# Kernel optimization log

Measured on AMD Instinct MI355X. Metric: run time of the kernel, lower is better.

The kernel has to match this reference:

```python
import jax, jax.numpy as jnp
import numpy as np

N, E, F_IN, HID, L, G = 50000, 800000, 128, 64, 3, 512
BN_EPS = 1e-5


def setup_inputs() -> dict:
    key = jax.random.key(0)
    ks = jax.random.split(key, 8)
    x = jax.random.normal(ks[0], (N, F_IN), dtype=jnp.float32)
    edge_index = jax.random.randint(ks[1], (2, E), 0, N, dtype=jnp.int32)
    batch = jnp.sort(jax.random.randint(ks[2], (N,), 0, G, dtype=jnp.int32))
    # params (Glorot-ish init for weights; BN init per module: gamma=1, beta=1e-4)
    W_feat = jax.random.normal(ks[3], (F_IN, HID), dtype=jnp.float32) / np.sqrt(F_IN)
    b_feat = jnp.zeros((HID,), jnp.float32)
    Ws = jax.random.normal(ks[4], (L, HID, HID), dtype=jnp.float32) / np.sqrt(HID)
    bs = jnp.zeros((L, HID), jnp.float32)
    bn_feat_g = jnp.ones((F_IN,), jnp.float32)
    bn_feat_b = jnp.full((F_IN,), 1e-4, jnp.float32)
    bn_g = jnp.ones((L, HID), jnp.float32)
    bn_b = jnp.full((L, HID), 1e-4, jnp.float32)
    return {"x": x, "edge_index": edge_index, "batch": batch,
            "bn_feat_g": bn_feat_g, "bn_feat_b": bn_feat_b,
            "W_feat": W_feat, "b_feat": b_feat,
            "bn_g": bn_g, "bn_b": bn_b, "Ws": Ws, "bs": bs}


def batch_norm(x, gamma, beta):
    # training-mode BatchNorm1d: biased variance over the node dimension
    mu = jnp.mean(x, axis=0)
    var = jnp.mean(jnp.square(x - mu), axis=0)
    return (x - mu) * jax.lax.rsqrt(var + BN_EPS) * gamma + beta


def gcn_conv(h, W, b, src, dst):
    # h: [N, d_in] -> linear then normalized gather-scatter with self-loops
    h = h @ W  # [N, d_out]
    n = h.shape[0]
    loop = jnp.arange(n, dtype=src.dtype)
    row = jnp.concatenate([src, loop])  # source (j)
    col = jnp.concatenate([dst, loop])  # target (i)
    w = jnp.ones(row.shape[0], h.dtype)
    deg = jax.ops.segment_sum(w, row, num_segments=n)  # PyG: deg over row
    dis = jnp.where(deg > 0, jax.lax.rsqrt(jnp.maximum(deg, 1.0)), 0.0)
    norm = dis[row] * w * dis[col]  # [E+N]
    out = jax.ops.segment_sum(norm[:, None] * h[row], col, num_segments=n)
    return out + b


def reference(x, edge_index, batch, bn_feat_g, bn_feat_b, W_feat, b_feat,
              bn_g, bn_b, Ws, bs):
    src, dst = edge_index[0], edge_index[1]
    h = batch_norm(x, bn_feat_g, bn_feat_b)
    h = jax.nn.relu(h @ W_feat + b_feat)  # conv_feat has gfn=True -> plain linear
    for i in range(L):
        h = batch_norm(h, bn_g[i], bn_b[i])
        h = jax.nn.relu(gcn_conv(h, Ws[i], bs[i], src, dst))
    graph_emb = jax.ops.segment_sum(h, batch, num_segments=G)  # global_add_pool
    return graph_emb
```

## Files before the change

### kernel.cpp

```cpp
#include <hip/hip_runtime.h>
#include <math.h>

#define HID 64
#define BN_EPS 1e-5f
#define NBMAX 256
#define NREP 64

typedef unsigned int uint;
typedef unsigned short ushort;


__device__ inline uint bf16pk(float a, float b) {
    uint ua = __builtin_bit_cast(uint, a);
    ua += 0x7fff + ((ua >> 16) & 1);
    uint ub = __builtin_bit_cast(uint, b);
    ub += 0x7fff + ((ub >> 16) & 1);
    return (ua >> 16) | (ub & 0xffff0000u);
}
__device__ inline float bfl(uint v) { return __builtin_bit_cast(float, v << 16); }
__device__ inline float bfh(uint v) { return __builtin_bit_cast(float, v & 0xffff0000u); }


__global__ __launch_bounds__(256) void k_hist_scan(const int* __restrict__ ei, int E, int NB, int N,
                                                   int* __restrict__ bcnt_d, int* __restrict__ bcnt_s,
                                                   int* __restrict__ done,
                                                   int* __restrict__ bbase_d, int* __restrict__ cursor_d,
                                                   int* __restrict__ bbase_s, int* __restrict__ cursor_s,
                                                   int* __restrict__ rowptr) {
    __shared__ int hd[256], hs[256];
    __shared__ int lastFlag;
    int t = threadIdx.x;
    hd[t] = 0; hs[t] = 0;
    __syncthreads();
    for (int e = blockIdx.x * 256 + t; e < E; e += gridDim.x * 256) {
        int src = ei[e], dst = ei[E + e];
        atomicAdd(&hs[src >> 8], 1);
        atomicAdd(&hd[dst >> 8], 1);
    }
    __syncthreads();
    if (t < NB) {
        if (hd[t]) atomicAdd(&bcnt_d[t], hd[t]);
        if (hs[t]) atomicAdd(&bcnt_s[t], hs[t]);
    }
    __threadfence();
    __syncthreads();
    if (t == 0) lastFlag = (atomicAdd(done, 1) == (int)gridDim.x - 1);
    __syncthreads();
    if (!lastFlag) return;
    int v = (t < NB) ? atomicAdd(&bcnt_d[t], 0) : 0;
    hd[t] = v; __syncthreads();
    for (int s = 1; s < 256; s <<= 1) { int u = (t >= s) ? hd[t - s] : 0; __syncthreads(); hd[t] += u; __syncthreads(); }
    int excl = hd[t] - v;
    if (t <= NB) bbase_d[t] = excl;
    if (t < NB) cursor_d[t] = excl;
    if (t == 0) rowptr[N] = E;
    __syncthreads();
    v = (t < NB) ? atomicAdd(&bcnt_s[t], 0) : 0;
    hs[t] = v; __syncthreads();
    for (int s = 1; s < 256; s <<= 1) { int u = (t >= s) ? hs[t - s] : 0; __syncthreads(); hs[t] += u; __syncthreads(); }
    excl = hs[t] - v;
    if (t <= NB) bbase_s[t] = excl;
    if (t < NB) cursor_s[t] = excl;
}

__global__ __launch_bounds__(256) void k_scatter_stats(const int* __restrict__ ei, int E, int NB, int SCB,
                                                       int* __restrict__ cursor_d, int* __restrict__ cursor_s,
                                                       uint* __restrict__ bedge, int* __restrict__ bsrc,
                                                       const float* __restrict__ X, int n,
                                                       float* __restrict__ stats) {
    __shared__ __align__(16) char smemraw[8192];
    int t = threadIdx.x;
    if ((int)blockIdx.x < SCB) {
        int* hd = (int*)smemraw;
        int* hs = hd + 256;
        int* curd = hs + 256;
        int* curs = curd + 256;
        int chunk = (E + SCB - 1) / SCB;
        int e0 = blockIdx.x * chunk;
        int e1 = min(e0 + chunk, E);
        if (t < NB) { hd[t] = 0; hs[t] = 0; }
        __syncthreads();
        for (int e = e0 + t; e < e1; e += 256) {
            int src = ei[e], dst = ei[E + e];
            atomicAdd(&hd[dst >> 8], 1);
            atomicAdd(&hs[src >> 8], 1);
        }
        __syncthreads();
        if (t < NB) {
            curd[t] = hd[t] ? atomicAdd(&cursor_d[t], hd[t]) : 0;
            curs[t] = hs[t] ? atomicAdd(&cursor_s[t], hs[t]) : 0;
        }
        __syncthreads();
        for (int e = e0 + t; e < e1; e += 256) {
            int src = ei[e], dst = ei[E + e];
            int pd = atomicAdd(&curd[dst >> 8], 1);
            bedge[pd] = ((uint)(dst & 255) << 16) | (uint)src;
            int ps = atomicAdd(&curs[src >> 8], 1);
            bsrc[ps] = src;
        }
    } else {
        int b = blockIdx.x - SCB;
        int SB = gridDim.x - SCB;
        float4* shs = (float4*)smemraw;
        float4* shq = shs + 256;
        int c4 = t & 31, rsub = t >> 5;
        float4 s = make_float4(0.f, 0.f, 0.f, 0.f);
        float4 q = make_float4(0.f, 0.f, 0.f, 0.f);
        for (int r = b * 8 + rsub; r < n; r += SB * 8) {
            float4 v = ((const float4*)X)[(size_t)r * 32 + c4];
            s.x += v.x; s.y += v.y; s.z += v.z; s.w += v.w;
            q.x = fmaf(v.x, v.x, q.x); q.y = fmaf(v.y, v.y, q.y);
            q.z = fmaf(v.z, v.z, q.z); q.w = fmaf(v.w, v.w, q.w);
        }
        shs[t] = s; shq[t] = q;
        __syncthreads();
        if (rsub == 0) {
            #pragma unroll
            for (int k = 1; k < 8; k++) {
                float4 a = shs[t + k * 32], bq = shq[t + k * 32];
                s.x += a.x; s.y += a.y; s.z += a.z; s.w += a.w;
                q.x += bq.x; q.y += bq.y; q.z += bq.z; q.w += bq.w;
            }
            float* sb = stats + ((int)blockIdx.x & (NREP - 1)) * 256;
            atomicAdd(&sb[4 * t + 0], s.x); atomicAdd(&sb[4 * t + 1], s.y);
            atomicAdd(&sb[4 * t + 2], s.z); atomicAdd(&sb[4 * t + 3], s.w);
            atomicAdd(&sb[128 + 4 * t + 0], q.x); atomicAdd(&sb[128 + 4 * t + 1], q.y);
            atomicAdd(&sb[128 + 4 * t + 2], q.z); atomicAdd(&sb[128 + 4 * t + 3], q.w);
        }
    }
}

__global__ __launch_bounds__(256) void k_build_csr_outdeg(
        const uint* __restrict__ bedge, const int* __restrict__ bbase_d,
        const int* __restrict__ bsrc, const int* __restrict__ bbase_s,
        int N, int NB,
        int* __restrict__ rowptr, int* __restrict__ eidx, float* __restrict__ dis) {
    __shared__ int h[256], off[256], cur[256];
    int t = threadIdx.x, b = blockIdx.x;
    if (b < NB) {
        int base = bbase_d[b], end = bbase_d[b + 1];
        h[t] = 0; __syncthreads();
        for (int p = base + t; p < end; p += 256)
            atomicAdd(&h[(int)(bedge[p] >> 16) & 255], 1);
        __syncthreads();
        off[t] = h[t]; __syncthreads();
        for (int s = 1; s < 256; s <<= 1) { int u = (t >= s) ? off[t - s] : 0; __syncthreads(); off[t] += u; __syncthreads(); }
        int excl = off[t] - h[t];
        int node = (b << 8) + t;
        if (node <= N) rowptr[node] = base + excl;
        cur[t] = excl; __syncthreads();
        for (int p = base + t; p < end; p += 256) {
            uint be = bedge[p];
            int bin = (int)(be >> 16) & 255;
            int pos = atomicAdd(&cur[bin], 1);
            eidx[base + pos] = (int)(be & 0xffffu);
        }
    } else {
        int b2 = b - NB;
        int base = bbase_s[b2], end = bbase_s[b2 + 1];
        h[t] = 0; __syncthreads();
        for (int p = base + t; p < end; p += 256) atomicAdd(&h[bsrc[p] & 255], 1);
        __syncthreads();
        int node = (b2 << 8) + t;
        if (node < N) dis[node] = rsqrtf((float)(h[t] + 1));
    }
}


template <int K, bool RELU, bool DIS, bool STATS, bool HASB>
__global__ __launch_bounds__(256) void k_gemm(const float* __restrict__ X, const float* __restrict__ W,
                                              const float* __restrict__ stats,
                                              const float* __restrict__ gamma, const float* __restrict__ beta,
                                              const float* __restrict__ bias0, const float* __restrict__ dis,
                                              float n_inv, void* __restrict__ out, int n,
                                              float* __restrict__ sout) {
    constexpr int KC = 64;
    constexpr int XS = 68;
    __shared__ float Xs[KC * XS];
    __shared__ float Wsm[KC * HID];
    __shared__ float As[128], Cs[128];

    int t = threadIdx.x;
    int tx = t & 15, ty = t >> 4;
    int row0 = blockIdx.x * 64;

    if (t < K) {
        float ssum = 0.f, qsum = 0.f;
        const float* sp = stats + t;
        #pragma unroll 8
        for (int r = 0; r < NREP; ++r) {
            ssum += sp[(size_t)r * 2 * K];
            qsum += sp[(size_t)r * 2 * K + K];
        }
        float mu = ssum * n_inv;
        float var = qsum * n_inv - mu * mu;
        float a = gamma[t] * rsqrtf(var + BN_EPS);
        As[t] = a;
        Cs[t] = beta[t] - mu * a;
    }
    __syncthreads();

    float acc[4][4];
    #pragma unroll
    for (int i = 0; i < 4; i++)
        #pragma unroll
        for (int j = 0; j < 4; j++) acc[i][j] = 0.f;
    float4 bp = make_float4(0.f, 0.f, 0.f, 0.f);

    for (int kc = 0; kc < K; kc += KC) {
        #pragma unroll
        for (int it = 0; it < 4; ++it) {
            int id = t + 256 * it;
            int r = id >> 4, c4 = id & 15;
            float4 v = make_float4(0.f, 0.f, 0.f, 0.f);
            if (row0 + r < n) v = *(const float4*)(X + (size_t)(row0 + r) * K + kc + 4 * c4);
            int kk = 4 * c4;
            Xs[(kk + 0) * XS + r] = v.x;
            Xs[(kk + 1) * XS + r] = v.y;
            Xs[(kk + 2) * XS + r] = v.z;
            Xs[(kk + 3) * XS + r] = v.w;
        }
        {
            const float4* wsrc = (const float4*)(W + (size_t)kc * HID);
            #pragma unroll
            for (int it = 0; it < 4; ++it) {
                int id = t + 256 * it;
                int kl = id >> 4;
                float4 raw = wsrc[id];
                float a = As[kc + kl], c = Cs[kc + kl];
                float4 sc;
                sc.x = a * raw.x; sc.y = a * raw.y; sc.z = a * raw.z; sc.w = a * raw.w;
                ((float4*)Wsm)[id] = sc;
                bp.x = fmaf(c, raw.x, bp.x);
                bp.y = fmaf(c, raw.y, bp.y);
                bp.z = fmaf(c, raw.z, bp.z);
                bp.w = fmaf(c, raw.w, bp.w);
            }
        }
        __syncthreads();
        #pragma unroll 8
        for (int k = 0; k < KC; ++k) {
            float4 xv = *(const float4*)&Xs[k * XS + 4 * ty];
            float4 wv = *(const float4*)&Wsm[k * HID + 4 * tx];
            acc[0][0] = fmaf(xv.x, wv.x, acc[0][0]);
            acc[0][1] = fmaf(xv.x, wv.y, acc[0][1]);
            acc[0][2] = fmaf(xv.x, wv.z, acc[0][2]);
            acc[0][3] = fmaf(xv.x, wv.w, acc[0][3]);
            acc[1][0] = fmaf(xv.y, wv.x, acc[1][0]);
            acc[1][1] = fmaf(xv.y, wv.y, acc[1][1]);
            acc[1][2] = fmaf(xv.y, wv.z, acc[1][2]);
            acc[1][3] = fmaf(xv.y, wv.w, acc[1][3]);
            acc[2][0] = fmaf(xv.z, wv.x, acc[2][0]);
            acc[2][1] = fmaf(xv.z, wv.y, acc[2][1]);
            acc[2][2] = fmaf(xv.z, wv.z, acc[2][2]);
            acc[2][3] = fmaf(xv.z, wv.w, acc[2][3]);
            acc[3][0] = fmaf(xv.w, wv.x, acc[3][0]);
            acc[3][1] = fmaf(xv.w, wv.y, acc[3][1]);
            acc[3][2] = fmaf(xv.w, wv.z, acc[3][2]);
            acc[3][3] = fmaf(xv.w, wv.w, acc[3][3]);
        }
        __syncthreads();
    }

    {
        float* redb = Xs + 2048;
        *(float4*)&redb[ty * 64 + 4 * tx] = bp;
        __syncthreads();
        if (t < 64) {
            float s = 0.f;
            #pragma unroll
            for (int k = 0; k < 16; ++k) s += redb[k * 64 + t];
            Xs[3072 + t] = s + (HASB ? bias0[t] : 0.f);
        }
        __syncthreads();
    }
    float4 bv = *(const float4*)&Xs[3072 + 4 * tx];

    float4 cs = make_float4(0.f, 0.f, 0.f, 0.f);
    float4 cq = make_float4(0.f, 0.f, 0.f, 0.f);
    #pragma unroll
    for (int i = 0; i < 4; ++i) {
        int row = row0 + 4 * ty + i;
        bool valid = row < n;
        float vx = acc[i][0] + bv.x, vy = acc[i][1] + bv.y;
        float vz = acc[i][2] + bv.z, vw = acc[i][3] + bv.w;
        if constexpr (DIS) {
            if (valid) {
                float d = dis[row];
                uint2 pk;
                pk.x = bf16pk(vx * d, vy * d);
                pk.y = bf16pk(vz * d, vw * d);
                *(uint2*)((ushort*)out + (size_t)row * HID + 4 * tx) = pk;
            }
        } else {
            float4 v;
            v.x = RELU ? fmaxf(vx, 0.f) : vx;
            v.y = RELU ? fmaxf(vy, 0.f) : vy;
            v.z = RELU ? fmaxf(vz, 0.f) : vz;
            v.w = RELU ? fmaxf(vw, 0.f) : vw;
            if (valid) {
                *(float4*)((float*)out + (size_t)row * HID + 4 * tx) = v;
                if constexpr (STATS) {
                    cs.x += v.x; cs.y += v.y; cs.z += v.z; cs.w += v.w;
                    cq.x = fmaf(v.x, v.x, cq.x); cq.y = fmaf(v.y, v.y, cq.y);
                    cq.z = fmaf(v.z, v.z, cq.z); cq.w = fmaf(v.w, v.w, cq.w);
                }
            }
        }
    }
    if constexpr (STATS) {
        __syncthreads();
        float* reds = Xs;
        float* redq = Xs + 1024;
        *(float4*)&reds[ty * 64 + 4 * tx] = cs;
        *(float4*)&redq[ty * 64 + 4 * tx] = cq;
        __syncthreads();
        if (t < 64) {
            float s = 0.f, q = 0.f;
            #pragma unroll
            for (int k = 0; k < 16; ++k) { s += reds[k * 64 + t]; q += redq[k * 64 + t]; }
            float* sb = sout + ((int)blockIdx.x & (NREP - 1)) * 128;
            atomicAdd(&sb[t], s);
            atomicAdd(&sb[64 + t], q);
        }
    }
}


template <bool POOL>
__global__ __launch_bounds__(256) void k_agg(const ushort* __restrict__ s, const int* __restrict__ rowptr,
                                             const int* __restrict__ eidx, const float* __restrict__ dis,
                                             const float* __restrict__ bias, float* __restrict__ out, int n,
                                             float* __restrict__ sout, const int* __restrict__ batch,
                                             float* __restrict__ pool_out) {
    __shared__ float shs[8 * 64];
    __shared__ float shq[8 * 64];
    __shared__ int ib[8];
    int t = threadIdx.x;
    int nl = t >> 5;
    int li = t & 31;
    int slot = li >> 3;
    int c = li & 7;
    int i = blockIdx.x * 8 + nl;
    const uint4* sp4 = (const uint4*)s;
    float a[8];
    #pragma unroll
    for (int k = 0; k < 8; ++k) a[k] = 0.f;
    bool valid = i < n;
    if (valid) {
        int qe = rowptr[i + 1];
        int q = rowptr[i] + slot;
        while (q < qe) {
            int qm = qe - 1;
            int q1 = q + 4, q2 = q + 8, q3 = q + 12;
            bool p1 = q1 < qe, p2 = q2 < qe, p3 = q3 < qe;
            int j0 = eidx[q];
            int j1 = eidx[min(q1, qm)];
            int j2 = eidx[min(q2, qm)];
            int j3 = eidx[min(q3, qm)];
            if (!p1) j1 = i;
            if (!p2) j2 = i;
            if (!p3) j3 = i;
            uint4 v0 = sp4[(size_t)j0 * 8 + c];
            uint4 v1 = sp4[(size_t)j1 * 8 + c];
            uint4 v2 = sp4[(size_t)j2 * 8 + c];
            uint4 v3 = sp4[(size_t)j3 * 8 + c];
            float m1 = p1 ? 1.f : 0.f;
            float m2 = p2 ? 1.f : 0.f;
            float m3 = p3 ? 1.f : 0.f;
            q += 16;
            a[0] += bfl(v0.x); a[1] += bfh(v0.x);
            a[2] += bfl(v0.y); a[3] += bfh(v0.y);
            a[4] += bfl(v0.z); a[5] += bfh(v0.z);
            a[6] += bfl(v0.w); a[7] += bfh(v0.w);
            a[0] = fmaf(m1, bfl(v1.x), a[0]); a[1] = fmaf(m1, bfh(v1.x), a[1]);
            a[2] = fmaf(m1, bfl(v1.y), a[2]); a[3] = fmaf(m1, bfh(v1.y), a[3]);
            a[4] = fmaf(m1, bfl(v1.z), a[4]); a[5] = fmaf(m1, bfh(v1.z), a[5]);
            a[6] = fmaf(m1, bfl(v1.w), a[6]); a[7] = fmaf(m1, bfh(v1.w), a[7]);
            a[0] = fmaf(m2, bfl(v2.x), a[0]); a[1] = fmaf(m2, bfh(v2.x), a[1]);
            a[2] = fmaf(m2, bfl(v2.y), a[2]); a[3] = fmaf(m2, bfh(v2.y), a[3]);
            a[4] = fmaf(m2, bfl(v2.z), a[4]); a[5] = fmaf(m2, bfh(v2.z), a[5]);
            a[6] = fmaf(m2, bfl(v2.w), a[6]); a[7] = fmaf(m2, bfh(v2.w), a[7]);
            a[0] = fmaf(m3, bfl(v3.x), a[0]); a[1] = fmaf(m3, bfh(v3.x), a[1]);
            a[2] = fmaf(m3, bfl(v3.y), a[2]); a[3] = fmaf(m3, bfh(v3.y), a[3]);
            a[4] = fmaf(m3, bfl(v3.z), a[4]); a[5] = fmaf(m3, bfh(v3.z), a[5]);
            a[6] = fmaf(m3, bfl(v3.w), a[6]); a[7] = fmaf(m3, bfh(v3.w), a[7]);
        }
    }
    #pragma unroll
    for (int k = 0; k < 8; ++k) a[k] += __shfl_xor(a[k], 8);
    #pragma unroll
    for (int k = 0; k < 8; ++k) a[k] += __shfl_xor(a[k], 16);

    if (li < 8) {
        float r[8];
        if (valid) {
            uint4 v = sp4[(size_t)i * 8 + c];
            a[0] += bfl(v.x); a[1] += bfh(v.x);
            a[2] += bfl(v.y); a[3] += bfh(v.y);
            a[4] += bfl(v.z); a[5] += bfh(v.z);
            a[6] += bfl(v.w); a[7] += bfh(v.w);
            float d = dis[i];
            float4 b0 = *(const float4*)(bias + 8 * c);
            float4 b1 = *(const float4*)(bias + 8 * c + 4);
            r[0] = fmaxf(fmaf(d, a[0], b0.x), 0.f);
            r[1] = fmaxf(fmaf(d, a[1], b0.y), 0.f);
            r[2] = fmaxf(fmaf(d, a[2], b0.z), 0.f);
            r[3] = fmaxf(fmaf(d, a[3], b0.w), 0.f);
            r[4] = fmaxf(fmaf(d, a[4], b1.x), 0.f);
            r[5] = fmaxf(fmaf(d, a[5], b1.y), 0.f);
            r[6] = fmaxf(fmaf(d, a[6], b1.z), 0.f);
            r[7] = fmaxf(fmaf(d, a[7], b1.w), 0.f);
            if constexpr (!POOL) {
                *(float4*)(out + (size_t)i * HID + 8 * c)     = make_float4(r[0], r[1], r[2], r[3]);
                *(float4*)(out + (size_t)i * HID + 8 * c + 4) = make_float4(r[4], r[5], r[6], r[7]);
            }
        } else {
            #pragma unroll
            for (int k = 0; k < 8; ++k) r[k] = 0.f;
        }
        #pragma unroll
        for (int k = 0; k < 8; ++k) shs[nl * 64 + 8 * c + k] = r[k];
        if constexpr (!POOL) {
            #pragma unroll
            for (int k = 0; k < 8; ++k) shq[nl * 64 + 8 * c + k] = r[k] * r[k];
        }
    }
    if constexpr (POOL) {
        if (li == 0) ib[nl] = valid ? batch[i] : -1;
    }
    __syncthreads();
    if (t < 64) {
        if constexpr (!POOL) {
            float ss = 0.f, qq = 0.f;
            #pragma unroll
            for (int k = 0; k < 8; ++k) { ss += shs[k * 64 + t]; qq += shq[k * 64 + t]; }
            float* sb = sout + ((int)blockIdx.x & (NREP - 1)) * 128;
            atomicAdd(&sb[t], ss);
            atomicAdd(&sb[64 + t], qq);
        } else {
            int g = ib[0];
            float run = shs[t];
            #pragma unroll
            for (int k = 1; k < 8; ++k) {
                int gk = ib[k];
                float v = shs[k * 64 + t];
                if (gk == g) {
                    run += v;
                } else {
                    if (g >= 0) atomicAdd(&pool_out[(size_t)g * HID + t], run);
                    g = gk; run = v;
                }
            }
            if (g >= 0) atomicAdd(&pool_out[(size_t)g * HID + t], run);
        }
    }
}


extern "C" void kernel_launch(void* const* d_in, const int* in_sizes, int n_in,
                              void* d_out, int out_size, void* d_ws, size_t ws_size,
                              hipStream_t stream) {
    const float* x     = (const float*)d_in[0];
    const int*   ei    = (const int*)d_in[1];
    const int*   batch = (const int*)d_in[2];
    const float* bnfg  = (const float*)d_in[3];
    const float* bnfb  = (const float*)d_in[4];
    const float* Wfeat = (const float*)d_in[5];
    const float* bfeat = (const float*)d_in[6];
    const float* bng   = (const float*)d_in[7];
    const float* bnb   = (const float*)d_in[8];
    const float* Ws    = (const float*)d_in[9];
    const float* bs    = (const float*)d_in[10];
    float* out = (float*)d_out;

    const int N   = in_sizes[2];
    const int E   = in_sizes[1] / 2;
    const int L   = in_sizes[9] / (HID * HID);
    const int NB  = (N + 255) >> 8;
    const int SCB = 256;
    const int SB  = 512;
    const int gG  = (N + 63) / 64;
    const int gA  = (N + 7) / 8;
    const float n_inv = 1.f / (float)N;

    char* w = (char*)d_ws;
    auto alloc = [&](size_t bytes) { char* p = w; w += (bytes + 255) & ~(size_t)255; return p; };
    int*   bcnt_d = (int*)alloc(256 * 4);
    int*   bcnt_s = (int*)alloc(256 * 4);
    int*   done   = (int*)alloc(256);
    float* statsX = (float*)alloc((size_t)NREP * 256 * 4);
    float* statsL = (float*)alloc((size_t)3 * NREP * 128 * 4);
    size_t zero_bytes = (size_t)(w - (char*)d_ws);
    int*   bbase_d  = (int*)alloc(257 * 4);
    int*   cursor_d = (int*)alloc(256 * 4);
    int*   bbase_s  = (int*)alloc(257 * 4);
    int*   cursor_s = (int*)alloc(256 * 4);
    int*   rowptr   = (int*)alloc(((size_t)N + 1) * 4);
    int*   eidx     = (int*)alloc((size_t)E * 4);
    float* dis      = (float*)alloc((size_t)N * 4);
    float* bufA     = (float*)alloc((size_t)N * HID * 4);
    ushort* bufB    = (ushort*)alloc((size_t)N * HID * 2);
    uint* bedge = (uint*)bufA;
    int*  bsrc  = (int*)bufB;

    hipMemsetAsync(d_ws, 0, zero_bytes, stream);
    hipMemsetAsync(d_out, 0, (size_t)out_size * sizeof(float), stream);

    k_hist_scan<<<512, 256, 0, stream>>>(ei, E, NB, N, bcnt_d, bcnt_s, done,
                                         bbase_d, cursor_d, bbase_s, cursor_s, rowptr);
    k_scatter_stats<<<SCB + SB, 256, 0, stream>>>(ei, E, NB, SCB, cursor_d, cursor_s,
                                                  bedge, bsrc, x, N, statsX);
    k_build_csr_outdeg<<<2 * NB, 256, 0, stream>>>(bedge, bbase_d, bsrc, bbase_s, N, NB,
                                                   rowptr, eidx, dis);

    k_gemm<128, true, false, true, true><<<gG, 256, 0, stream>>>(
        x, Wfeat, statsX, bnfg, bnfb, bfeat, nullptr, n_inv, (void*)bufA, N, statsL);

    for (int l = 0; l < L; ++l) {
        k_gemm<64, false, true, false, false><<<gG, 256, 0, stream>>>(
            bufA, Ws + (size_t)l * HID * HID, statsL + (size_t)l * NREP * 128,
            bng + (size_t)l * HID, bnb + (size_t)l * HID,
            nullptr, dis, n_inv, (void*)bufB, N, nullptr);
        if (l < L - 1) {
            k_agg<false><<<gA, 256, 0, stream>>>(bufB, rowptr, eidx, dis, bs + (size_t)l * HID,
                                                 bufA, N, statsL + (size_t)(l + 1) * NREP * 128,
                                                 nullptr, nullptr);
        } else {
            k_agg<true><<<gA, 256, 0, stream>>>(bufB, rowptr, eidx, dis, bs + (size_t)l * HID,
                                                nullptr, N, nullptr, batch, out);
        }
    }
}
```

Measured before the change: 287.9 us.

## Build CSR with per-node atomic degrees, decoupled-lookback scan, and atomic fill

Replaces the two-level bucketed counting sort (bucket histogram, bucket scatter, per-bucket local sort) with a simpler CSR build. Per-node degrees now come from global atomics, a single-pass scan with decoupled lookback produces rowptr, cursor and dis, and an atomic-cursor fill writes eidx. This cuts the kernel count and the intermediate bedge/bsrc passes, at the cost of many contended global atomics. Edge order inside each row also becomes nondeterministic, so the aggregation's floating-point summation order can vary between runs.

```diff
diff --git a/kernel.cpp b/kernel.cpp
--- a/kernel.cpp
+++ b/kernel.cpp
@@ -3,7 +3,6 @@
 
 #define HID 64
 #define BN_EPS 1e-5f
-#define NBMAX 256
 #define NREP 64
 
 typedef unsigned int uint;
@@ -21,86 +20,22 @@
 __device__ inline float bfh(uint v) { return __builtin_bit_cast(float, v & 0xffff0000u); }
 
 
-__global__ __launch_bounds__(256) void k_hist_scan(const int* __restrict__ ei, int E, int NB, int N,
-                                                   int* __restrict__ bcnt_d, int* __restrict__ bcnt_s,
-                                                   int* __restrict__ done,
-                                                   int* __restrict__ bbase_d, int* __restrict__ cursor_d,
-                                                   int* __restrict__ bbase_s, int* __restrict__ cursor_s,
-                                                   int* __restrict__ rowptr) {
-    __shared__ int hd[256], hs[256];
-    __shared__ int lastFlag;
-    int t = threadIdx.x;
-    hd[t] = 0; hs[t] = 0;
-    __syncthreads();
-    for (int e = blockIdx.x * 256 + t; e < E; e += gridDim.x * 256) {
-        int src = ei[e], dst = ei[E + e];
-        atomicAdd(&hs[src >> 8], 1);
-        atomicAdd(&hd[dst >> 8], 1);
-    }
-    __syncthreads();
-    if (t < NB) {
-        if (hd[t]) atomicAdd(&bcnt_d[t], hd[t]);
-        if (hs[t]) atomicAdd(&bcnt_s[t], hs[t]);
-    }
-    __threadfence();
-    __syncthreads();
-    if (t == 0) lastFlag = (atomicAdd(done, 1) == (int)gridDim.x - 1);
-    __syncthreads();
-    if (!lastFlag) return;
-    int v = (t < NB) ? atomicAdd(&bcnt_d[t], 0) : 0;
-    hd[t] = v; __syncthreads();
-    for (int s = 1; s < 256; s <<= 1) { int u = (t >= s) ? hd[t - s] : 0; __syncthreads(); hd[t] += u; __syncthreads(); }
-    int excl = hd[t] - v;
-    if (t <= NB) bbase_d[t] = excl;
-    if (t < NB) cursor_d[t] = excl;
-    if (t == 0) rowptr[N] = E;
-    __syncthreads();
-    v = (t < NB) ? atomicAdd(&bcnt_s[t], 0) : 0;
-    hs[t] = v; __syncthreads();
-    for (int s = 1; s < 256; s <<= 1) { int u = (t >= s) ? hs[t - s] : 0; __syncthreads(); hs[t] += u; __syncthreads(); }
-    excl = hs[t] - v;
-    if (t <= NB) bbase_s[t] = excl;
-    if (t < NB) cursor_s[t] = excl;
-}
-
-__global__ __launch_bounds__(256) void k_scatter_stats(const int* __restrict__ ei, int E, int NB, int SCB,
-                                                       int* __restrict__ cursor_d, int* __restrict__ cursor_s,
-                                                       uint* __restrict__ bedge, int* __restrict__ bsrc,
-                                                       const float* __restrict__ X, int n,
-                                                       float* __restrict__ stats) {
+__global__ __launch_bounds__(256) void k_deg_stats(const int* __restrict__ ei, int E, int DB,
+                                                   int* __restrict__ deg_d, int* __restrict__ deg_s,
+                                                   const float* __restrict__ X, int n,
+                                                   float* __restrict__ stats) {
     __shared__ __align__(16) char smemraw[8192];
     int t = threadIdx.x;
-    if ((int)blockIdx.x < SCB) {
-        int* hd = (int*)smemraw;
-        int* hs = hd + 256;
-        int* curd = hs + 256;
-        int* curs = curd + 256;
-        int chunk = (E + SCB - 1) / SCB;
-        int e0 = blockIdx.x * chunk;
-        int e1 = min(e0 + chunk, E);
-        if (t < NB) { hd[t] = 0; hs[t] = 0; }
-        __syncthreads();
-        for (int e = e0 + t; e < e1; e += 256) {
+    if ((int)blockIdx.x < DB) {
+        int stride = DB * 256;
+        for (int e = blockIdx.x * 256 + t; e < E; e += stride) {
             int src = ei[e], dst = ei[E + e];
-            atomicAdd(&hd[dst >> 8], 1);
-            atomicAdd(&hs[src >> 8], 1);
-        }
-        __syncthreads();
-        if (t < NB) {
-            curd[t] = hd[t] ? atomicAdd(&cursor_d[t], hd[t]) : 0;
-            curs[t] = hs[t] ? atomicAdd(&cursor_s[t], hs[t]) : 0;
-        }
-        __syncthreads();
-        for (int e = e0 + t; e < e1; e += 256) {
-            int src = ei[e], dst = ei[E + e];
-            int pd = atomicAdd(&curd[dst >> 8], 1);
-            bedge[pd] = ((uint)(dst & 255) << 16) | (uint)src;
-            int ps = atomicAdd(&curs[src >> 8], 1);
-            bsrc[ps] = src;
+            atomicAdd(&deg_s[src], 1);
+            atomicAdd(&deg_d[dst], 1);
         }
     } else {
-        int b = blockIdx.x - SCB;
-        int SB = gridDim.x - SCB;
+        int b = blockIdx.x - DB;
+        int SB = gridDim.x - DB;
         float4* shs = (float4*)smemraw;
         float4* shq = shs + 256;
         int c4 = t & 31, rsub = t >> 5;
@@ -130,39 +65,80 @@
     }
 }
 
-__global__ __launch_bounds__(256) void k_build_csr_outdeg(
-        const uint* __restrict__ bedge, const int* __restrict__ bbase_d,
-        const int* __restrict__ bsrc, const int* __restrict__ bbase_s,
-        int N, int NB,
-        int* __restrict__ rowptr, int* __restrict__ eidx, float* __restrict__ dis) {
-    __shared__ int h[256], off[256], cur[256];
+
+__global__ __launch_bounds__(256) void k_scan_dis(const int* __restrict__ deg_d,
+                                                  const int* __restrict__ deg_s,
+                                                  int N, int E,
+                                                  int* __restrict__ rowptr, int* __restrict__ cursor,
+                                                  float* __restrict__ dis,
+                                                  int* __restrict__ aggr, int* __restrict__ flag) {
+    __shared__ int sh[256];
+    __shared__ int s_base;
     int t = threadIdx.x, b = blockIdx.x;
-    if (b < NB) {
-        int base = bbase_d[b], end = bbase_d[b + 1];
-        h[t] = 0; __syncthreads();
-        for (int p = base + t; p < end; p += 256)
-            atomicAdd(&h[(int)(bedge[p] >> 16) & 255], 1);
-        __syncthreads();
-        off[t] = h[t]; __syncthreads();
-        for (int s = 1; s < 256; s <<= 1) { int u = (t >= s) ? off[t - s] : 0; __syncthreads(); off[t] += u; __syncthreads(); }
-        int excl = off[t] - h[t];
-        int node = (b << 8) + t;
-        if (node <= N) rowptr[node] = base + excl;
-        cur[t] = excl; __syncthreads();
-        for (int p = base + t; p < end; p += 256) {
-            uint be = bedge[p];
-            int bin = (int)(be >> 16) & 255;
-            int pos = atomicAdd(&cur[bin], 1);
-            eidx[base + pos] = (int)(be & 0xffffu);
-        }
+    int base_el = b * 1024 + t * 4;
+
+    int4 ds = *(const int4*)(deg_s + base_el);
+    float4 dv;
+    dv.x = rsqrtf((float)(ds.x + 1)); dv.y = rsqrtf((float)(ds.y + 1));
+    dv.z = rsqrtf((float)(ds.z + 1)); dv.w = rsqrtf((float)(ds.w + 1));
+    if (base_el + 3 < N) *(float4*)(dis + base_el) = dv;
+    else {
+        if (base_el + 0 < N) dis[base_el + 0] = dv.x;
+        if (base_el + 1 < N) dis[base_el + 1] = dv.y;
+        if (base_el + 2 < N) dis[base_el + 2] = dv.z;
+        if (base_el + 3 < N) dis[base_el + 3] = dv.w;
+    }
+
+    int4 d = *(const int4*)(deg_d + base_el);
+    int s3 = d.x + d.y + d.z + d.w;
+    sh[t] = s3;
+    __syncthreads();
+    for (int off = 1; off < 256; off <<= 1) {
+        int u = (t >= off) ? sh[t - off] : 0;
+        __syncthreads();
+        sh[t] += u;
+        __syncthreads();
+    }
+    int excl_thread = sh[t] - s3;
+    int block_total = sh[255];
+
+    if (t == 0) {
+        s_base = 0;
+        atomicExch(&aggr[b], block_total);
+        __threadfence();
+        atomicExch(&flag[b], 1);
+    }
+    __syncthreads();
+    int lb = 0;
+    for (int p = t; p < b; p += 256) {
+        while (atomicAdd(&flag[p], 0) == 0) { __builtin_amdgcn_s_sleep(2); }
+        lb += atomicAdd(&aggr[p], 0);
+    }
+    if (lb) atomicAdd(&s_base, lb);
+    __syncthreads();
+
+    int base = s_base + excl_thread;
+    int r0 = base, r1 = r0 + d.x, r2 = r1 + d.y, r3 = r2 + d.z;
+    if (base_el + 3 < N) {
+        *(int4*)(rowptr + base_el) = make_int4(r0, r1, r2, r3);
+        *(int4*)(cursor + base_el) = make_int4(r0, r1, r2, r3);
     } else {
-        int b2 = b - NB;
-        int base = bbase_s[b2], end = bbase_s[b2 + 1];
-        h[t] = 0; __syncthreads();
-        for (int p = base + t; p < end; p += 256) atomicAdd(&h[bsrc[p] & 255], 1);
-        __syncthreads();
-        int node = (b2 << 8) + t;
-        if (node < N) dis[node] = rsqrtf((float)(h[t] + 1));
+        if (base_el + 0 < N) { rowptr[base_el + 0] = r0; cursor[base_el + 0] = r0; }
+        if (base_el + 1 < N) { rowptr[base_el + 1] = r1; cursor[base_el + 1] = r1; }
+        if (base_el + 2 < N) { rowptr[base_el + 2] = r2; cursor[base_el + 2] = r2; }
+        if (base_el + 3 < N) { rowptr[base_el + 3] = r3; cursor[base_el + 3] = r3; }
+    }
+    if (b == (int)gridDim.x - 1 && t == 255) rowptr[N] = E;
+}
+
+
+__global__ __launch_bounds__(256) void k_fill(const int* __restrict__ ei, int E,
+                                              int* __restrict__ cursor, int* __restrict__ eidx) {
+    int stride = gridDim.x * 256;
+    for (int e = blockIdx.x * 256 + threadIdx.x; e < E; e += stride) {
+        int src = ei[e], dst = ei[E + e];
+        int pos = atomicAdd(&cursor[dst], 1);
+        eidx[pos] = src;
     }
 }
 
@@ -477,42 +453,36 @@
     const int N   = in_sizes[2];
     const int E   = in_sizes[1] / 2;
     const int L   = in_sizes[9] / (HID * HID);
-    const int NB  = (N + 255) >> 8;
-    const int SCB = 256;
+    const int DB  = 512;
     const int SB  = 512;
+    const int SC  = (N + 1023) / 1024;
+    const int FB  = 1024;
     const int gG  = (N + 63) / 64;
     const int gA  = (N + 7) / 8;
     const float n_inv = 1.f / (float)N;
 
     char* w = (char*)d_ws;
     auto alloc = [&](size_t bytes) { char* p = w; w += (bytes + 255) & ~(size_t)255; return p; };
-    int*   bcnt_d = (int*)alloc(256 * 4);
-    int*   bcnt_s = (int*)alloc(256 * 4);
-    int*   done   = (int*)alloc(256);
+    int*   deg_d  = (int*)alloc(((size_t)N + 1024) * 4);
+    int*   deg_s  = (int*)alloc(((size_t)N + 1024) * 4);
+    int*   aggr   = (int*)alloc(256 * 4);
+    int*   flag   = (int*)alloc(256 * 4);
     float* statsX = (float*)alloc((size_t)NREP * 256 * 4);
     float* statsL = (float*)alloc((size_t)3 * NREP * 128 * 4);
     size_t zero_bytes = (size_t)(w - (char*)d_ws);
-    int*   bbase_d  = (int*)alloc(257 * 4);
-    int*   cursor_d = (int*)alloc(256 * 4);
-    int*   bbase_s  = (int*)alloc(257 * 4);
-    int*   cursor_s = (int*)alloc(256 * 4);
-    int*   rowptr   = (int*)alloc(((size_t)N + 1) * 4);
-    int*   eidx     = (int*)alloc((size_t)E * 4);
-    float* dis      = (float*)alloc((size_t)N * 4);
-    float* bufA     = (float*)alloc((size_t)N * HID * 4);
-    ushort* bufB    = (ushort*)alloc((size_t)N * HID * 2);
-    uint* bedge = (uint*)bufA;
-    int*  bsrc  = (int*)bufB;
+    int*   rowptr = (int*)alloc(((size_t)N + 1024) * 4);
+    int*   cursor = (int*)alloc(((size_t)N + 1024) * 4);
+    int*   eidx   = (int*)alloc((size_t)E * 4);
+    float* dis    = (float*)alloc((size_t)N * 4);
+    float* bufA   = (float*)alloc((size_t)N * HID * 4);
+    ushort* bufB  = (ushort*)alloc((size_t)N * HID * 2);
 
     hipMemsetAsync(d_ws, 0, zero_bytes, stream);
     hipMemsetAsync(d_out, 0, (size_t)out_size * sizeof(float), stream);
 
-    k_hist_scan<<<512, 256, 0, stream>>>(ei, E, NB, N, bcnt_d, bcnt_s, done,
-                                         bbase_d, cursor_d, bbase_s, cursor_s, rowptr);
-    k_scatter_stats<<<SCB + SB, 256, 0, stream>>>(ei, E, NB, SCB, cursor_d, cursor_s,
-                                                  bedge, bsrc, x, N, statsX);
-    k_build_csr_outdeg<<<2 * NB, 256, 0, stream>>>(bedge, bbase_d, bsrc, bbase_s, N, NB,
-                                                   rowptr, eidx, dis);
+    k_deg_stats<<<DB + SB, 256, 0, stream>>>(ei, E, DB, deg_d, deg_s, x, N, statsX);
+    k_scan_dis<<<SC, 256, 0, stream>>>(deg_d, deg_s, N, E, rowptr, cursor, dis, aggr, flag);
+    k_fill<<<FB, 256, 0, stream>>>(ei, E, cursor, eidx);
 
     k_gemm<128, true, false, true, true><<<gG, 256, 0, stream>>>(
         x, Wfeat, statsX, bnfg, bnfb, bfeat, nullptr, n_inv, (void*)bufA, N, statsL);
```

After: 345.4 us. 20.0% more time.

## Fuse input BN stats into histogram pass and first GEMM into edge scatter

Applied to the files above, without the earlier changes.

Moves the input-feature BatchNorm statistics reduction into the edge histogram/scan kernel, and runs the first feature GEMM in the same launch as the edge bucket scatter, using disjoint block ranges. This cuts one kernel launch and lets the independent graph-preprocessing and dense work overlap on the GPU. To allow the overlap, bedge/bsrc get their own workspace buffers instead of aliasing bufA/bufB, which costs extra memory. The combined kernel also uses more shared memory per block, which may lower occupancy for the scatter blocks.

```diff
diff --git a/kernel.cpp b/kernel.cpp
--- a/kernel.cpp
+++ b/kernel.cpp
@@ -3,7 +3,6 @@
 
 #define HID 64
 #define BN_EPS 1e-5f
-#define NBMAX 256
 #define NREP 64
 
 typedef unsigned int uint;
@@ -21,86 +20,53 @@
 __device__ inline float bfh(uint v) { return __builtin_bit_cast(float, v & 0xffff0000u); }
 
 
-__global__ __launch_bounds__(256) void k_hist_scan(const int* __restrict__ ei, int E, int NB, int N,
-                                                   int* __restrict__ bcnt_d, int* __restrict__ bcnt_s,
-                                                   int* __restrict__ done,
-                                                   int* __restrict__ bbase_d, int* __restrict__ cursor_d,
-                                                   int* __restrict__ bbase_s, int* __restrict__ cursor_s,
-                                                   int* __restrict__ rowptr) {
-    __shared__ int hd[256], hs[256];
+__global__ __launch_bounds__(256) void k_hist_scan_stats(
+        const int* __restrict__ ei, int E, int NB, int N, int HB,
+        int* __restrict__ bcnt_d, int* __restrict__ bcnt_s, int* __restrict__ done,
+        int* __restrict__ bbase_d, int* __restrict__ cursor_d,
+        int* __restrict__ bbase_s, int* __restrict__ cursor_s,
+        int* __restrict__ rowptr,
+        const float* __restrict__ X, int n, float* __restrict__ stats) {
+    __shared__ __align__(16) char smemraw[8192];
     __shared__ int lastFlag;
     int t = threadIdx.x;
-    hd[t] = 0; hs[t] = 0;
-    __syncthreads();
-    for (int e = blockIdx.x * 256 + t; e < E; e += gridDim.x * 256) {
-        int src = ei[e], dst = ei[E + e];
-        atomicAdd(&hs[src >> 8], 1);
-        atomicAdd(&hd[dst >> 8], 1);
-    }
-    __syncthreads();
-    if (t < NB) {
-        if (hd[t]) atomicAdd(&bcnt_d[t], hd[t]);
-        if (hs[t]) atomicAdd(&bcnt_s[t], hs[t]);
-    }
-    __threadfence();
-    __syncthreads();
-    if (t == 0) lastFlag = (atomicAdd(done, 1) == (int)gridDim.x - 1);
-    __syncthreads();
-    if (!lastFlag) return;
-    int v = (t < NB) ? atomicAdd(&bcnt_d[t], 0) : 0;
-    hd[t] = v; __syncthreads();
-    for (int s = 1; s < 256; s <<= 1) { int u = (t >= s) ? hd[t - s] : 0; __syncthreads(); hd[t] += u; __syncthreads(); }
-    int excl = hd[t] - v;
-    if (t <= NB) bbase_d[t] = excl;
-    if (t < NB) cursor_d[t] = excl;
-    if (t == 0) rowptr[N] = E;
-    __syncthreads();
-    v = (t < NB) ? atomicAdd(&bcnt_s[t], 0) : 0;
-    hs[t] = v; __syncthreads();
-    for (int s = 1; s < 256; s <<= 1) { int u = (t >= s) ? hs[t - s] : 0; __syncthreads(); hs[t] += u; __syncthreads(); }
-    excl = hs[t] - v;
-    if (t <= NB) bbase_s[t] = excl;
-    if (t < NB) cursor_s[t] = excl;
-}
-
-__global__ __launch_bounds__(256) void k_scatter_stats(const int* __restrict__ ei, int E, int NB, int SCB,
-                                                       int* __restrict__ cursor_d, int* __restrict__ cursor_s,
-                                                       uint* __restrict__ bedge, int* __restrict__ bsrc,
-                                                       const float* __restrict__ X, int n,
-                                                       float* __restrict__ stats) {
-    __shared__ __align__(16) char smemraw[8192];
-    int t = threadIdx.x;
-    if ((int)blockIdx.x < SCB) {
+    if ((int)blockIdx.x < HB) {
         int* hd = (int*)smemraw;
         int* hs = hd + 256;
-        int* curd = hs + 256;
-        int* curs = curd + 256;
-        int chunk = (E + SCB - 1) / SCB;
-        int e0 = blockIdx.x * chunk;
-        int e1 = min(e0 + chunk, E);
-        if (t < NB) { hd[t] = 0; hs[t] = 0; }
-        __syncthreads();
-        for (int e = e0 + t; e < e1; e += 256) {
+        hd[t] = 0; hs[t] = 0;
+        __syncthreads();
+        for (int e = blockIdx.x * 256 + t; e < E; e += HB * 256) {
             int src = ei[e], dst = ei[E + e];
+            atomicAdd(&hs[src >> 8], 1);
             atomicAdd(&hd[dst >> 8], 1);
-            atomicAdd(&hs[src >> 8], 1);
         }
         __syncthreads();
         if (t < NB) {
-            curd[t] = hd[t] ? atomicAdd(&cursor_d[t], hd[t]) : 0;
-            curs[t] = hs[t] ? atomicAdd(&cursor_s[t], hs[t]) : 0;
-        }
-        __syncthreads();
-        for (int e = e0 + t; e < e1; e += 256) {
-            int src = ei[e], dst = ei[E + e];
-            int pd = atomicAdd(&curd[dst >> 8], 1);
-            bedge[pd] = ((uint)(dst & 255) << 16) | (uint)src;
-            int ps = atomicAdd(&curs[src >> 8], 1);
-            bsrc[ps] = src;
-        }
+            if (hd[t]) atomicAdd(&bcnt_d[t], hd[t]);
+            if (hs[t]) atomicAdd(&bcnt_s[t], hs[t]);
+        }
+        __threadfence();
+        __syncthreads();
+        if (t == 0) lastFlag = (atomicAdd(done, 1) == HB - 1);
+        __syncthreads();
+        if (!lastFlag) return;
+        int v = (t < NB) ? atomicAdd(&bcnt_d[t], 0) : 0;
+        hd[t] = v; __syncthreads();
+        for (int s = 1; s < 256; s <<= 1) { int u = (t >= s) ? hd[t - s] : 0; __syncthreads(); hd[t] += u; __syncthreads(); }
+        int excl = hd[t] - v;
+        if (t <= NB) bbase_d[t] = excl;
+        if (t < NB) cursor_d[t] = excl;
+        if (t == 0) rowptr[N] = E;
+        __syncthreads();
+        v = (t < NB) ? atomicAdd(&bcnt_s[t], 0) : 0;
+        hs[t] = v; __syncthreads();
+        for (int s = 1; s < 256; s <<= 1) { int u = (t >= s) ? hs[t - s] : 0; __syncthreads(); hs[t] += u; __syncthreads(); }
+        excl = hs[t] - v;
+        if (t <= NB) bbase_s[t] = excl;
+        if (t < NB) cursor_s[t] = excl;
     } else {
-        int b = blockIdx.x - SCB;
-        int SB = gridDim.x - SCB;
+        int b = blockIdx.x - HB;
+        int SB = gridDim.x - HB;
         float4* shs = (float4*)smemraw;
         float4* shq = shs + 256;
         int c4 = t & 31, rsub = t >> 5;
@@ -130,50 +96,14 @@
     }
 }
 
-__global__ __launch_bounds__(256) void k_build_csr_outdeg(
-        const uint* __restrict__ bedge, const int* __restrict__ bbase_d,
-        const int* __restrict__ bsrc, const int* __restrict__ bbase_s,
-        int N, int NB,
-        int* __restrict__ rowptr, int* __restrict__ eidx, float* __restrict__ dis) {
-    __shared__ int h[256], off[256], cur[256];
-    int t = threadIdx.x, b = blockIdx.x;
-    if (b < NB) {
-        int base = bbase_d[b], end = bbase_d[b + 1];
-        h[t] = 0; __syncthreads();
-        for (int p = base + t; p < end; p += 256)
-            atomicAdd(&h[(int)(bedge[p] >> 16) & 255], 1);
-        __syncthreads();
-        off[t] = h[t]; __syncthreads();
-        for (int s = 1; s < 256; s <<= 1) { int u = (t >= s) ? off[t - s] : 0; __syncthreads(); off[t] += u; __syncthreads(); }
-        int excl = off[t] - h[t];
-        int node = (b << 8) + t;
-        if (node <= N) rowptr[node] = base + excl;
-        cur[t] = excl; __syncthreads();
-        for (int p = base + t; p < end; p += 256) {
-            uint be = bedge[p];
-            int bin = (int)(be >> 16) & 255;
-            int pos = atomicAdd(&cur[bin], 1);
-            eidx[base + pos] = (int)(be & 0xffffu);
-        }
-    } else {
-        int b2 = b - NB;
-        int base = bbase_s[b2], end = bbase_s[b2 + 1];
-        h[t] = 0; __syncthreads();
-        for (int p = base + t; p < end; p += 256) atomicAdd(&h[bsrc[p] & 255], 1);
-        __syncthreads();
-        int node = (b2 << 8) + t;
-        if (node < N) dis[node] = rsqrtf((float)(h[t] + 1));
-    }
-}
-
 
 template <int K, bool RELU, bool DIS, bool STATS, bool HASB>
-__global__ __launch_bounds__(256) void k_gemm(const float* __restrict__ X, const float* __restrict__ W,
-                                              const float* __restrict__ stats,
-                                              const float* __restrict__ gamma, const float* __restrict__ beta,
-                                              const float* __restrict__ bias0, const float* __restrict__ dis,
-                                              float n_inv, void* __restrict__ out, int n,
-                                              float* __restrict__ sout) {
+__device__ __forceinline__ void gemm_body(const float* __restrict__ X, const float* __restrict__ W,
+                                          const float* __restrict__ stats,
+                                          const float* __restrict__ gamma, const float* __restrict__ beta,
+                                          const float* __restrict__ bias0, const float* __restrict__ dis,
+                                          float n_inv, void* __restrict__ out, int n,
+                                          float* __restrict__ sout, int bx) {
     constexpr int KC = 64;
     constexpr int XS = 68;
     __shared__ float Xs[KC * XS];
@@ -182,7 +112,7 @@
 
     int t = threadIdx.x;
     int tx = t & 15, ty = t >> 4;
-    int row0 = blockIdx.x * 64;
+    int row0 = bx * 64;
 
     if (t < K) {
         float ssum = 0.f, qsum = 0.f;
@@ -319,10 +249,100 @@
             float s = 0.f, q = 0.f;
             #pragma unroll
             for (int k = 0; k < 16; ++k) { s += reds[k * 64 + t]; q += redq[k * 64 + t]; }
-            float* sb = sout + ((int)blockIdx.x & (NREP - 1)) * 128;
+            float* sb = sout + ((int)bx & (NREP - 1)) * 128;
             atomicAdd(&sb[t], s);
             atomicAdd(&sb[64 + t], q);
         }
+    }
+}
+
+template <int K, bool RELU, bool DIS, bool STATS, bool HASB>
+__global__ __launch_bounds__(256) void k_gemm(const float* __restrict__ X, const float* __restrict__ W,
+                                              const float* __restrict__ stats,
+                                              const float* __restrict__ gamma, const float* __restrict__ beta,
+                                              const float* __restrict__ bias0, const float* __restrict__ dis,
+                                              float n_inv, void* __restrict__ out, int n,
+                                              float* __restrict__ sout) {
+    gemm_body<K, RELU, DIS, STATS, HASB>(X, W, stats, gamma, beta, bias0, dis, n_inv, out, n, sout,
+                                         (int)blockIdx.x);
+}
+
+
+__global__ __launch_bounds__(256) void k_scatter_gemm(
+        const int* __restrict__ ei, int E, int NB, int SCB,
+        int* __restrict__ cursor_d, int* __restrict__ cursor_s,
+        uint* __restrict__ bedge, int* __restrict__ bsrc,
+        const float* __restrict__ X, const float* __restrict__ W,
+        const float* __restrict__ stats,
+        const float* __restrict__ gamma, const float* __restrict__ beta,
+        const float* __restrict__ bias0,
+        float n_inv, void* __restrict__ out, int n, float* __restrict__ sout) {
+    int t = threadIdx.x;
+    if ((int)blockIdx.x < SCB) {
+        __shared__ int hd[256], hs[256], curd[256], curs[256];
+        int chunk = (E + SCB - 1) / SCB;
+        int e0 = blockIdx.x * chunk;
+        int e1 = min(e0 + chunk, E);
+        if (t < NB) { hd[t] = 0; hs[t] = 0; }
+        __syncthreads();
+        for (int e = e0 + t; e < e1; e += 256) {
+            int src = ei[e], dst = ei[E + e];
+            atomicAdd(&hd[dst >> 8], 1);
+            atomicAdd(&hs[src >> 8], 1);
+        }
+        __syncthreads();
+        if (t < NB) {
+            curd[t] = hd[t] ? atomicAdd(&cursor_d[t], hd[t]) : 0;
+            curs[t] = hs[t] ? atomicAdd(&cursor_s[t], hs[t]) : 0;
+        }
+        __syncthreads();
+        for (int e = e0 + t; e < e1; e += 256) {
+            int src = ei[e], dst = ei[E + e];
+            int pd = atomicAdd(&curd[dst >> 8], 1);
+            bedge[pd] = ((uint)(dst & 255) << 16) | (uint)src;
+            int ps = atomicAdd(&curs[src >> 8], 1);
+            bsrc[ps] = src;
+        }
+    } else {
+        gemm_body<128, true, false, true, true>(X, W, stats, gamma, beta, bias0, nullptr,
+                                                n_inv, out, n, sout, (int)blockIdx.x - SCB);
+    }
+}
+
+
+__global__ __launch_bounds__(256) void k_build_csr_outdeg(
+        const uint* __restrict__ bedge, const int* __restrict__ bbase_d,
+        const int* __restrict__ bsrc, const int* __restrict__ bbase_s,
+        int N, int NB,
+        int* __restrict__ rowptr, int* __restrict__ eidx, float* __restrict__ dis) {
+    __shared__ int h[256], off[256], cur[256];
+    int t = threadIdx.x, b = blockIdx.x;
+    if (b < NB) {
+        int base = bbase_d[b], end = bbase_d[b + 1];
+        h[t] = 0; __syncthreads();
+        for (int p = base + t; p < end; p += 256)
+            atomicAdd(&h[(int)(bedge[p] >> 16) & 255], 1);
+        __syncthreads();
+        off[t] = h[t]; __syncthreads();
+        for (int s = 1; s < 256; s <<= 1) { int u = (t >= s) ? off[t - s] : 0; __syncthreads(); off[t] += u; __syncthreads(); }
+        int excl = off[t] - h[t];
+        int node = (b << 8) + t;
+        if (node <= N) rowptr[node] = base + excl;
+        cur[t] = excl; __syncthreads();
+        for (int p = base + t; p < end; p += 256) {
+            uint be = bedge[p];
+            int bin = (int)(be >> 16) & 255;
+            int pos = atomicAdd(&cur[bin], 1);
+            eidx[base + pos] = (int)(be & 0xffffu);
+        }
+    } else {
+        int b2 = b - NB;
+        int base = bbase_s[b2], end = bbase_s[b2 + 1];
+        h[t] = 0; __syncthreads();
+        for (int p = base + t; p < end; p += 256) atomicAdd(&h[bsrc[p] & 255], 1);
+        __syncthreads();
+        int node = (b2 << 8) + t;
+        if (node < N) dis[node] = rsqrtf((float)(h[t] + 1));
     }
 }
 
@@ -478,8 +498,9 @@
     const int E   = in_sizes[1] / 2;
     const int L   = in_sizes[9] / (HID * HID);
     const int NB  = (N + 255) >> 8;
+    const int HB  = 128;
+    const int SB  = 512;
     const int SCB = 256;
-    const int SB  = 512;
     const int gG  = (N + 63) / 64;
     const int gA  = (N + 7) / 8;
     const float n_inv = 1.f / (float)N;
@@ -501,21 +522,20 @@
     float* dis      = (float*)alloc((size_t)N * 4);
     float* bufA     = (float*)alloc((size_t)N * HID * 4);
     ushort* bufB    = (ushort*)alloc((size_t)N * HID * 2);
-    uint* bedge = (uint*)bufA;
-    int*  bsrc  = (int*)bufB;
+    uint*  bedge    = (uint*)alloc((size_t)E * 4);
+    int*   bsrc     = (int*)alloc((size_t)E * 4);
 
     hipMemsetAsync(d_ws, 0, zero_bytes, stream);
     hipMemsetAsync(d_out, 0, (size_t)out_size * sizeof(float), stream);
 
-    k_hist_scan<<<512, 256, 0, stream>>>(ei, E, NB, N, bcnt_d, bcnt_s, done,
-                                         bbase_d, cursor_d, bbase_s, cursor_s, rowptr);
-    k_scatter_stats<<<SCB + SB, 256, 0, stream>>>(ei, E, NB, SCB, cursor_d, cursor_s,
-                                                  bedge, bsrc, x, N, statsX);
+    k_hist_scan_stats<<<HB + SB, 256, 0, stream>>>(ei, E, NB, N, HB, bcnt_d, bcnt_s, done,
+                                                   bbase_d, cursor_d, bbase_s, cursor_s, rowptr,
+                                                   x, N, statsX);
+    k_scatter_gemm<<<SCB + gG, 256, 0, stream>>>(ei, E, NB, SCB, cursor_d, cursor_s, bedge, bsrc,
+                                                 x, Wfeat, statsX, bnfg, bnfb, bfeat,
+                                                 n_inv, (void*)bufA, N, statsL);
     k_build_csr_outdeg<<<2 * NB, 256, 0, stream>>>(bedge, bbase_d, bsrc, bbase_s, N, NB,
                                                    rowptr, eidx, dis);
-
-    k_gemm<128, true, false, true, true><<<gG, 256, 0, stream>>>(
-        x, Wfeat, statsX, bnfg, bnfb, bfeat, nullptr, n_inv, (void*)bufA, N, statsL);
 
     for (int l = 0; l < L; ++l) {
         k_gemm<64, false, true, false, false><<<gG, 256, 0, stream>>>(
```

New measurement: 260.4 us. -9.6%, faster.
